# Optimization experiments

Measured on AMD Instinct MI355X. Metric: run time of the kernel, lower is better.

Reference implementation:

```python
import jax, jax.numpy as jnp
import numpy as np

# Production-scale GBDT ensemble config
B = 32768          # batch
T = 512            # num_trees
D = 8              # max_tree_depth
F = 512            # n_features
C = 1              # n_classes
PAD = T * 2 ** (D - 1)  # padded per-level width (level l uses first T*2**l slots)


def setup_inputs() -> dict:
    key = jax.random.key(0)
    ks = jax.random.split(key, 6)
    x = jax.random.normal(ks[0], (B, F), jnp.float32)
    root_nodes = jax.random.randint(ks[1], (T,), 0, F, jnp.int32)
    root_biases = jax.random.normal(ks[2], (T,), jnp.float32)
    tree_indices = (2 * jnp.arange(T)).astype(jnp.int32)
    # nodes_lv[l-1, t*2**l + j] = feature index of node j of tree t at depth l
    nodes_lv = jax.random.randint(ks[3], (D - 1, PAD), 0, F, jnp.int32)
    # biases_lv holds -(-threshold) = thresholds (already negated twice as in torch module)
    biases_lv = jax.random.normal(ks[4], (D - 1, PAD), jnp.float32)
    leaf_nodes = jax.random.normal(ks[5], (T * 2 ** D, C), jnp.float32)
    return dict(x=x, root_nodes=root_nodes, root_biases=root_biases,
                tree_indices=tree_indices, nodes_lv=nodes_lv,
                biases_lv=biases_lv, leaf_nodes=leaf_nodes)


def reference(x, root_nodes, root_biases, tree_indices, nodes_lv, biases_lv, leaf_nodes):
    # Root level: compare selected feature per tree against root threshold.
    prev = (x[:, root_nodes] >= root_biases[None, :]).astype(jnp.int32)  # (B, T)
    prev = prev + tree_indices[None, :]  # encodes t*2 + bit
    # Walk remaining D-1 levels; prev in [0, T*2**l) at level l.
    n_levels = nodes_lv.shape[0]
    for l in range(n_levels):
        feat_idx = nodes_lv[l][prev]                      # (B, T) feature ids
        feats = jnp.take_along_axis(x, feat_idx, axis=1)  # (B, T) gathered features
        bit = (feats >= biases_lv[l][prev]).astype(jnp.int32)
        prev = 2 * prev + bit
    # Final leaf lookup: (B, T, C)
    return leaf_nodes[prev]
```

## Files before the change

kernel.cpp:

```cpp
#include <hip/hip_runtime.h>


#define BB 32768
#define TT 512
#define FF 512
#define PADW 65536
#define ROWS 32
#define THREADS 1024
#define TPW 32
#define XSS 515

#define PT0_OFF 0
#define PT1_OFF 1024
#define PT2_OFF 5120
#define PT3_OFF 21504
#define N_REC   87040

__global__ __launch_bounds__(256) void build_tables_kernel(
    const int*   __restrict__ nodes_lv,
    const float* __restrict__ biases_lv,
    const float* __restrict__ leaf_nodes,
    int4*        __restrict__ ws16)
{
    const int i = blockIdx.x * 256 + threadIdx.x;
    if (i >= N_REC) return;

    int l, p, off;
    if (i < PT1_OFF)      { l = 0; off = PT0_OFF; }
    else if (i < PT2_OFF) { l = 2; off = PT1_OFF; }
    else if (i < PT3_OFF) { l = 4; off = PT2_OFF; }
    else {
        p = i - PT3_OFF;
        const int   f  = nodes_lv[6 * PADW + p];
        const float b  = biases_lv[6 * PADW + p];
        const float lL = leaf_nodes[2 * p];
        const float lR = leaf_nodes[2 * p + 1];
        ws16[i] = make_int4(f, __float_as_int(b),
                            __float_as_int(lL), __float_as_int(lR));
        return;
    }
    p = i - off;
    const int   f0 = nodes_lv[l * PADW + p];
    const float b0 = biases_lv[l * PADW + p];
    const int   fL = nodes_lv[(l + 1) * PADW + 2 * p];
    const int   fR = nodes_lv[(l + 1) * PADW + 2 * p + 1];
    const float bL = biases_lv[(l + 1) * PADW + 2 * p];
    const float bR = biases_lv[(l + 1) * PADW + 2 * p + 1];
    ws16[i] = make_int4(f0 | (fL << 10) | (fR << 20), __float_as_int(b0),
                        __float_as_int(bL), __float_as_int(bR));
}

#define PAIR_STAGE(REC, P)                                                    \
    {                                                                         \
        const int   fp = (REC).x;                                             \
        const float xp = xrow[fp & 1023];                                     \
        const float xl = xrow[(fp >> 10) & 1023];                             \
        const float xh = xrow[(fp >> 20) & 1023];                             \
        const bool  g0 = xp >= __int_as_float((REC).y);                       \
        const float xc = g0 ? xh : xl;                                        \
        const float hc = g0 ? __int_as_float((REC).w) : __int_as_float((REC).z); \
        const bool  g1 = xc >= hc;                                            \
        (P) = 4 * (P) + 2 * (int)g0 + (int)g1;                                \
    }

__global__ __launch_bounds__(THREADS) void gbdt_walk_kernel(
    const float* __restrict__ x,
    const int*   __restrict__ root_nodes,
    const float* __restrict__ root_biases,
    const int4*  __restrict__ ws16,
    float*       __restrict__ out)
{
    __shared__ float xs[ROWS * XSS];
    __shared__ int4  pt0[1024];
    __shared__ int4  pt1[4096];
    __shared__ int2  rt[512];

    const int tid = threadIdx.x;
    const int b0  = blockIdx.x * ROWS;

    const float4* __restrict__ xr = (const float4*)(x + (size_t)b0 * FF);
    #pragma unroll
    for (int i = 0; i < (ROWS * FF / 4) / THREADS; ++i) {
        int fidx = i * THREADS + tid;
        int r = fidx >> 7, c4 = fidx & 127;
        float4 v = xr[fidx];
        float* d = &xs[r * XSS + (c4 << 2)];
        d[0] = v.x; d[1] = v.y; d[2] = v.z; d[3] = v.w;
    }
    #pragma unroll
    for (int i = 0; i < 5; ++i) {
        int idx = i * THREADS + tid;
        if (idx < 5120) {
            int4 v = ws16[idx];
            if (idx < 1024) pt0[idx] = v;
            else            pt1[idx - 1024] = v;
        }
    }
    if (tid < 512)
        rt[tid] = make_int2(root_nodes[tid], __float_as_int(root_biases[tid]));
    __syncthreads();

    const int wv   = tid >> 6;
    const int lane = tid & 63;
    const int row  = lane & 31;
    const int g    = lane >> 5;
    const int tb   = wv * TPW;
    const float* __restrict__ xrow = &xs[row * XSS];
    float* __restrict__ orow = out + (size_t)(b0 + row) * TT;

    #pragma unroll
    for (int s = 0; s < TPW / 8; ++s) {
        const int tbase = tb + 8 * s + 4 * g;
        int p[4];

        #pragma unroll
        for (int c = 0; c < 4; ++c) {
            const int t = tbase + c;
            const int2 rn = rt[t];
            const bool rb = xrow[rn.x] >= __int_as_float(rn.y);
            p[c] = 2 * t + (int)rb;
        }
        {
            int4 r0[4];
            #pragma unroll
            for (int c = 0; c < 4; ++c) r0[c] = pt0[p[c]];
            #pragma unroll
            for (int c = 0; c < 4; ++c) PAIR_STAGE(r0[c], p[c]);
        }
        {
            int4 r1[4];
            #pragma unroll
            for (int c = 0; c < 4; ++c) r1[c] = pt1[p[c]];
            #pragma unroll
            for (int c = 0; c < 4; ++c) PAIR_STAGE(r1[c], p[c]);
        }
        {
            int4 r2[4];
            #pragma unroll
            for (int c = 0; c < 4; ++c) r2[c] = ws16[PT2_OFF + p[c]];
            #pragma unroll
            for (int c = 0; c < 4; ++c) PAIR_STAGE(r2[c], p[c]);
        }
        int4 r3[4];
        #pragma unroll
        for (int c = 0; c < 4; ++c) r3[c] = ws16[PT3_OFF + p[c]];
        float v[4];
        #pragma unroll
        for (int c = 0; c < 4; ++c) {
            const bool gg = xrow[r3[c].x] >= __int_as_float(r3[c].y);
            v[c] = gg ? __int_as_float(r3[c].w) : __int_as_float(r3[c].z);
        }
        *(float4*)&orow[tbase] = make_float4(v[0], v[1], v[2], v[3]);
    }
}

__global__ __launch_bounds__(THREADS) void gbdt_walk_fallback(
    const float* __restrict__ x,
    const int*   __restrict__ root_nodes,
    const float* __restrict__ root_biases,
    const int*   __restrict__ nodes_lv,
    const float* __restrict__ biases_lv,
    const float* __restrict__ leaf_nodes,
    float*       __restrict__ out)
{
    __shared__ float xs[ROWS * XSS];
    const int tid = threadIdx.x;
    const int b0  = blockIdx.x * ROWS;
    const float4* __restrict__ xr = (const float4*)(x + (size_t)b0 * FF);
    #pragma unroll
    for (int i = 0; i < (ROWS * FF / 4) / THREADS; ++i) {
        int fidx = i * THREADS + tid;
        int r = fidx >> 7, c4 = fidx & 127;
        float4 v = xr[fidx];
        float* d = &xs[r * XSS + (c4 << 2)];
        d[0] = v.x; d[1] = v.y; d[2] = v.z; d[3] = v.w;
    }
    __syncthreads();
    const int wv   = tid >> 6;
    const int lane = tid & 63;
    const int row  = lane & 31;
    const int g    = lane >> 5;
    const int tb   = wv * TPW;
    const float* __restrict__ xrow = &xs[row * XSS];
    float* __restrict__ orow = out + (size_t)(b0 + row) * TT;
    #pragma unroll
    for (int s = 0; s < TPW / 2; ++s) {
        const int t = tb + 2 * s + g;
        int p = 2 * t + (xrow[root_nodes[t]] >= root_biases[t] ? 1 : 0);
        #pragma unroll
        for (int l = 0; l < 7; ++l) {
            const int   f = nodes_lv[l * PADW + p];
            const float h = biases_lv[l * PADW + p];
            p = 2 * p + (xrow[f] >= h ? 1 : 0);
        }
        orow[t] = leaf_nodes[p];
    }
}

extern "C" void kernel_launch(void* const* d_in, const int* in_sizes, int n_in,
                              void* d_out, int out_size, void* d_ws, size_t ws_size,
                              hipStream_t stream) {
    const float* x            = (const float*)d_in[0];
    const int*   root_nodes   = (const int*)  d_in[1];
    const float* root_biases  = (const float*)d_in[2];
    const int*   nodes_lv     = (const int*)  d_in[4];
    const float* biases_lv    = (const float*)d_in[5];
    const float* leaf_nodes   = (const float*)d_in[6];
    float*       out          = (float*)d_out;

    dim3 grid(BB / ROWS);
    dim3 block(THREADS);

    if (ws_size >= (size_t)N_REC * 16) {
        int4* ws16 = (int4*)d_ws;
        build_tables_kernel<<<(N_REC + 255) / 256, 256, 0, stream>>>(
            nodes_lv, biases_lv, leaf_nodes, ws16);
        gbdt_walk_kernel<<<grid, block, 0, stream>>>(
            x, root_nodes, root_biases, ws16, out);
    } else {
        gbdt_walk_fallback<<<grid, block, 0, stream>>>(
            x, root_nodes, root_biases, nodes_lv, biases_lv, leaf_nodes, out);
    }
}
```

Before: 72.00 us.

## Batch global table loads across all tree groups and resolve pair stages lazily

The walk loop is reorganized so that for all 16 trees per thread, the shared-memory levels are resolved first and the level-4/5 global record loads are issued together. All level-6 global loads are then issued before any leaf comparisons, putting more independent global loads in flight to hide latency. The pair stage now reads only the chosen child's feature instead of both children, saving one LDS read per stage but adding a dependent read. A launch_bounds occupancy hint is added. More live int4 registers per thread may lower occupancy or cause spills.

Result: faster. 67.91 us (-5.7%).

```diff
diff --git a/kernel.cpp b/kernel.cpp
--- a/kernel.cpp
+++ b/kernel.cpp
@@ -50,20 +50,17 @@
                         __float_as_int(bL), __float_as_int(bR));
 }
 
-#define PAIR_STAGE(REC, P)                                                    \
+#define PAIR_RESOLVE(REC, P)                                                  \
     {                                                                         \
         const int   fp = (REC).x;                                             \
-        const float xp = xrow[fp & 1023];                                     \
-        const float xl = xrow[(fp >> 10) & 1023];                             \
-        const float xh = xrow[(fp >> 20) & 1023];                             \
-        const bool  g0 = xp >= __int_as_float((REC).y);                       \
-        const float xc = g0 ? xh : xl;                                        \
-        const float hc = g0 ? __int_as_float((REC).w) : __int_as_float((REC).z); \
-        const bool  g1 = xc >= hc;                                            \
+        const bool  g0 = xrow[fp & 1023] >= __int_as_float((REC).y);          \
+        const int   f1 = g0 ? ((fp >> 20) & 1023) : ((fp >> 10) & 1023);      \
+        const float h1 = g0 ? __int_as_float((REC).w) : __int_as_float((REC).z); \
+        const bool  g1 = xrow[f1] >= h1;                                      \
         (P) = 4 * (P) + 2 * (int)g0 + (int)g1;                                \
     }
 
-__global__ __launch_bounds__(THREADS) void gbdt_walk_kernel(
+__global__ __launch_bounds__(THREADS, 4) void gbdt_walk_kernel(
     const float* __restrict__ x,
     const int*   __restrict__ root_nodes,
     const float* __restrict__ root_biases,
@@ -108,47 +105,46 @@
     const float* __restrict__ xrow = &xs[row * XSS];
     float* __restrict__ orow = out + (size_t)(b0 + row) * TT;
 
-    #pragma unroll
-    for (int s = 0; s < TPW / 8; ++s) {
+    int  p4[16];
+    int4 r2[4][4];
+
+    #pragma unroll
+    for (int s = 0; s < 4; ++s) {
         const int tbase = tb + 8 * s + 4 * g;
-        int p[4];
-
         #pragma unroll
         for (int c = 0; c < 4; ++c) {
             const int t = tbase + c;
             const int2 rn = rt[t];
-            const bool rb = xrow[rn.x] >= __int_as_float(rn.y);
-            p[c] = 2 * t + (int)rb;
-        }
-        {
-            int4 r0[4];
-            #pragma unroll
-            for (int c = 0; c < 4; ++c) r0[c] = pt0[p[c]];
-            #pragma unroll
-            for (int c = 0; c < 4; ++c) PAIR_STAGE(r0[c], p[c]);
-        }
-        {
-            int4 r1[4];
-            #pragma unroll
-            for (int c = 0; c < 4; ++c) r1[c] = pt1[p[c]];
-            #pragma unroll
-            for (int c = 0; c < 4; ++c) PAIR_STAGE(r1[c], p[c]);
-        }
-        {
-            int4 r2[4];
-            #pragma unroll
-            for (int c = 0; c < 4; ++c) r2[c] = ws16[PT2_OFF + p[c]];
-            #pragma unroll
-            for (int c = 0; c < 4; ++c) PAIR_STAGE(r2[c], p[c]);
-        }
-        int4 r3[4];
-        #pragma unroll
-        for (int c = 0; c < 4; ++c) r3[c] = ws16[PT3_OFF + p[c]];
+            int p = 2 * t + (xrow[rn.x] >= __int_as_float(rn.y) ? 1 : 0);
+            const int4 r0 = pt0[p];
+            PAIR_RESOLVE(r0, p);
+            const int4 r1 = pt1[p];
+            PAIR_RESOLVE(r1, p);
+            p4[4 * s + c] = p;
+            r2[s][c] = ws16[PT2_OFF + p];
+        }
+    }
+
+    int4 r3[4][4];
+    #pragma unroll
+    for (int s = 0; s < 4; ++s) {
+        #pragma unroll
+        for (int c = 0; c < 4; ++c) {
+            int p = p4[4 * s + c];
+            PAIR_RESOLVE(r2[s][c], p);
+            r3[s][c] = ws16[PT3_OFF + p];
+        }
+    }
+
+    #pragma unroll
+    for (int s = 0; s < 4; ++s) {
+        const int tbase = tb + 8 * s + 4 * g;
         float v[4];
         #pragma unroll
         for (int c = 0; c < 4; ++c) {
-            const bool gg = xrow[r3[c].x] >= __int_as_float(r3[c].y);
-            v[c] = gg ? __int_as_float(r3[c].w) : __int_as_float(r3[c].z);
+            const int4 r = r3[s][c];
+            const bool gg = xrow[r.x] >= __int_as_float(r.y);
+            v[c] = gg ? __int_as_float(r.w) : __int_as_float(r.z);
         }
         *(float4*)&orow[tbase] = make_float4(v[0], v[1], v[2], v[3]);
     }
```
